# Kernel tuning notes

Measured on AMD Instinct MI355X. Metric: run time of the kernel, lower is better.

The kernel has to match this reference:

```python
import jax, jax.numpy as jnp
import numpy as np
import math

B, T, C = 2, 2048, 1024
H = 16
D = C // H  # 64


def alibi_slopes(n_heads):
    # n_heads is a power of 2 here (16): slopes[i] = start * ratio**i with start==ratio==2**(-8/n)
    start = 2.0 ** (-(2.0 ** (-(math.log2(n_heads) - 3))))
    return jnp.asarray([start * start ** i for i in range(n_heads)], dtype=jnp.float32)


def setup_inputs() -> dict:
    key = jax.random.key(0)
    ks = jax.random.split(key, 6)
    x = jax.random.normal(ks[0], (B, T, C), dtype=jnp.float32)
    W_attn = jax.random.normal(ks[1], (C, 3 * C), dtype=jnp.float32) * 0.02
    b_attn = jnp.zeros((3 * C,), dtype=jnp.float32)
    W_proj = jax.random.normal(ks[2], (C, C), dtype=jnp.float32) * 0.02
    b_proj = jnp.zeros((C,), dtype=jnp.float32)
    temperature = jnp.ones((1,), dtype=jnp.float32) * 2.0
    return {"x": x, "W_attn": W_attn, "b_attn": b_attn,
            "W_proj": W_proj, "b_proj": b_proj, "temperature": temperature}


def reference(x, W_attn, b_attn, W_proj, b_proj, temperature):
    Bc, Tc, Cc = x.shape
    qkv = x @ W_attn + b_attn                      # (B, T, 3C)
    q, k, v = jnp.split(qkv, 3, axis=-1)
    q = q.reshape(Bc, Tc, H, D)
    k = k.reshape(Bc, Tc, H, D)
    v = v.reshape(Bc, Tc, H, D)
    scale = 1.0 / math.sqrt(D)
    att = jnp.einsum('bqhd,bkhd->bhqk', q, k) * scale  # (B, H, T, T)
    att = att / temperature                            # learnable temperature
    # ALiBi bias with causal mask (-inf above diagonal)
    pos = jnp.arange(Tc, dtype=jnp.float32)
    rel = pos[None, :] - pos[:, None]                  # (T, T): memory - context
    slopes = alibi_slopes(H)
    bias = slopes[:, None, None] * rel[None, :, :]
    causal = pos[None, :] <= pos[:, None]              # (T, T) lower-triangular
    bias = jnp.where(causal[None, :, :], bias, -jnp.inf)
    att = att + bias[None, :, :, :]
    w = jax.nn.softmax(att, axis=-1)
    y = jnp.einsum('bhqk,bkhd->bqhd', w, v).reshape(Bc, Tc, Cc)
    return y @ W_proj + b_proj
```

## Files before the change

### kernel.cpp

```cpp
#include <hip/hip_runtime.h>
#include <math.h>

#define B_ 2
#define T_ 2048
#define C_ 1024
#define H_ 16
#define D_ 64
#define M_ (B_*T_)

typedef unsigned short u16;
typedef unsigned int u32;
typedef __attribute__((ext_vector_type(8))) short short8;
typedef __attribute__((ext_vector_type(4))) float f32x4;

__device__ inline u16 f2bf(float f){
  union { float f; unsigned u; } v; v.f = f;
  unsigned r = (v.u + 0x7FFF + ((v.u >> 16) & 1)) >> 16;
  return (u16)r;
}

__device__ inline void gload_lds16(const void* g, void* l){
  __builtin_amdgcn_global_load_lds(
      (const __attribute__((address_space(1))) unsigned*)g,
      (__attribute__((address_space(3))) unsigned*)l, 16, 0, 0);
}

__device__ inline int swzb(int row, int chunk){
  return (row << 7) | ((chunk ^ (row & 7)) << 4);
}

__global__ void k_cvt_x(const float* __restrict__ x, u16* __restrict__ xb){
  int i = (blockIdx.x * 256 + threadIdx.x) * 8;
  float4 a = *(const float4*)(x + i);
  float4 b = *(const float4*)(x + i + 4);
  short8 o;
  o[0] = (short)f2bf(a.x); o[1] = (short)f2bf(a.y);
  o[2] = (short)f2bf(a.z); o[3] = (short)f2bf(a.w);
  o[4] = (short)f2bf(b.x); o[5] = (short)f2bf(b.y);
  o[6] = (short)f2bf(b.z); o[7] = (short)f2bf(b.w);
  *(short8*)(xb + i) = o;
}

__global__ void k_transW(const float* __restrict__ W, u16* __restrict__ Wt, int K, int N){
  __shared__ float t[32][33];
  int bn = blockIdx.x * 32, bk = blockIdx.y * 32;
  int tx = threadIdx.x, ty = threadIdx.y;
  #pragma unroll
  for (int i = 0; i < 32; i += 8)
    t[ty + i][tx] = W[(size_t)(bk + ty + i) * N + bn + tx];
  __syncthreads();
  #pragma unroll
  for (int i = 0; i < 32; i += 8)
    Wt[(size_t)(bn + ty + i) * K + bk + tx] = f2bf(t[tx][ty + i]);
}

__global__ void k_transV(const u16* __restrict__ v, u16* __restrict__ vt){
  __shared__ u16 t[32][33];
  int bh = blockIdx.z;
  int t0 = blockIdx.x * 32, d0 = blockIdx.y * 32;
  int tx = threadIdx.x, ty = threadIdx.y;
  const u16* vs = v + (size_t)bh * T_ * D_;
  u16* vd = vt + (size_t)bh * T_ * D_;
  #pragma unroll
  for (int i = 0; i < 32; i += 8)
    t[ty + i][tx] = vs[(size_t)(t0 + ty + i) * D_ + d0 + tx];
  __syncthreads();
  #pragma unroll
  for (int i = 0; i < 32; i += 8)
    vd[(size_t)(d0 + ty + i) * T_ + t0 + tx] = t[tx][ty + i];
}

template<int EPI>
__launch_bounds__(256, 2)
__global__ void k_gemm(const u16* __restrict__ A, const u16* __restrict__ Bt,
                       const float* __restrict__ bias, float* __restrict__ outF,
                       u16* __restrict__ oq, u16* __restrict__ ok, u16* __restrict__ ov,
                       int M, int N, int K){
  __shared__ u16 lA[128 * 32];
  __shared__ u16 lB[128 * 32];
  int tid = threadIdx.x, lane = tid & 63, wv = tid >> 6;
  int bm = blockIdx.y * 128, bn = blockIdx.x * 128;
  int wr = (wv >> 1) * 64, wc = (wv & 1) * 64;
  f32x4 acc[4][4] = {};

  const u16* Ab = A + (size_t)(bm + wv * 32 + (lane >> 2)) * K + (lane & 3) * 8;
  const u16* Bb = Bt + (size_t)(bn + wv * 32 + (lane >> 2)) * K + (lane & 3) * 8;
  u16* lAd = &lA[wv * 1024];
  u16* lBd = &lB[wv * 1024];
  int ar = wr + (lane & 15);
  int br = wc + (lane & 15);
  int kc = (lane >> 4) * 8;

  for (int k0 = 0; k0 < K; k0 += 32){
    gload_lds16(Ab + k0, lAd);
    gload_lds16(Ab + k0 + (size_t)16 * K, lAd + 512);
    gload_lds16(Bb + k0, lBd);
    gload_lds16(Bb + k0 + (size_t)16 * K, lBd + 512);
    __syncthreads();
    short8 afr[4], bfr[4];
    #pragma unroll
    for (int m = 0; m < 4; m++) afr[m] = *(const short8*)&lA[(ar + m * 16) * 32 + kc];
    #pragma unroll
    for (int n = 0; n < 4; n++) bfr[n] = *(const short8*)&lB[(br + n * 16) * 32 + kc];
    #pragma unroll
    for (int m = 0; m < 4; m++)
      #pragma unroll
      for (int n = 0; n < 4; n++)
        acc[m][n] = __builtin_amdgcn_mfma_f32_16x16x32_bf16(afr[m], bfr[n], acc[m][n], 0, 0, 0);
    __syncthreads();
  }

  if (EPI == 1){
    #pragma unroll
    for (int m = 0; m < 4; m++){
      int gmB = bm + wr + m * 16 + ((lane >> 4) << 2);
      #pragma unroll
      for (int n = 0; n < 4; n++){
        int gn = bn + wc + n * 16 + (lane & 15);
        float bia = bias[gn];
        #pragma unroll
        for (int j = 0; j < 4; j++)
          outF[(size_t)(gmB + j) * N + gn] = acc[m][n][j] + bia;
      }
    }
  } else {
    #pragma unroll
    for (int m = 0; m < 4; m++){
      int gmB = bm + wr + m * 16 + ((lane >> 4) << 2);
      #pragma unroll
      for (int n = 0; n < 4; n++){
        int gn = bn + wc + n * 16 + (lane & 15);
        float bia = bias[gn];
        int part = gn >> 10;
        int col = gn & 1023;
        int h = col >> 6, d = col & 63;
        u16* dst = (part == 0) ? oq : (part == 1) ? ok : ov;
        #pragma unroll
        for (int j = 0; j < 4; j++){
          int gm = gmB + j;
          int b = gm >> 11, t = gm & 2047;
          dst[((size_t)(b * H_ + h) * T_ + t) * D_ + d] = f2bf(acc[m][n][j] + bia);
        }
      }
    }
  }
}

__launch_bounds__(256, 2)
__global__ void k_attn(const u16* __restrict__ q, const u16* __restrict__ k,
                       const u16* __restrict__ vt, u16* __restrict__ y,
                       const float* __restrict__ tempPtr){
  __shared__ u16 lK[64 * 64];
  __shared__ u16 lV[64 * 64];
  __shared__ u16 lP[4][32 * 64];
  const float LOG2E = 1.44269504089f;
  int tid = threadIdx.x, lane = tid & 63, wv = tid >> 6;
  int g = lane >> 4, c = lane & 15;
  int bh = blockIdx.x, h = bh & (H_ - 1), b = bh >> 4;
  int yy = blockIdx.y;
  int qt = (yy & 1) ? ((yy - 1) >> 1) : (15 - (yy >> 1));
  int q0 = qt * 128;
  int qb = q0 + wv * 32;
  float scl2 = LOG2E / (8.0f * tempPtr[0]);
  float slope2 = exp2f(-0.5f * (float)(h + 1)) * LOG2E;
  const u16* qp = q + (size_t)bh * T_ * D_;
  const u16* kp = k + (size_t)bh * T_ * D_;
  const u16* vp = vt + (size_t)bh * T_ * D_;
  char* lKc = (char*)lK;
  char* lVc = (char*)lV;
  char* lPw = (char*)lP[wv];

  short8 qf[2][2];
  #pragma unroll
  for (int m = 0; m < 2; m++)
    #pragma unroll
    for (int ks = 0; ks < 2; ks++)
      qf[m][ks] = *(const short8*)&qp[(size_t)(qb + m * 16 + c) * D_ + ks * 32 + g * 8];

  float boff[16];
  #pragma unroll
  for (int n = 0; n < 4; n++)
    #pragma unroll
    for (int r = 0; r < 4; r++)
      boff[n * 4 + r] = slope2 * (float)(n * 16 + g * 4 + r);
  float sq[2] = { slope2 * (float)(qb + c), slope2 * (float)(qb + 16 + c) };

  float mrun[2] = { -1e30f, -1e30f }, lrun[2] = { 0.f, 0.f };
  f32x4 acco[2][4] = {};

  int sr = tid >> 2, sc = tid & 3;
  const u16* gK = kp + (size_t)sr * D_ + sc * 16;
  const u16* gV = vp + (size_t)sr * T_ + sc * 16;
  short8 rk0, rk1, rv0, rv1;

  int ntiles = (q0 >> 6) + 2;
  int wqmax = qb + 31;

  rk0 = *(const short8*)(gK);     rk1 = *(const short8*)(gK + 8);
  rv0 = *(const short8*)(gV);     rv1 = *(const short8*)(gV + 8);

  for (int t = 0; t < ntiles; t++){
    int kv0 = t << 6;
    __syncthreads();
    *(short8*)(lKc + swzb(sr, sc * 2))     = rk0;
    *(short8*)(lKc + swzb(sr, sc * 2 + 1)) = rk1;
    *(short8*)(lVc + swzb(sr, sc * 2))     = rv0;
    *(short8*)(lVc + swzb(sr, sc * 2 + 1)) = rv1;
    __syncthreads();
    if (t + 1 < ntiles){
      rk0 = *(const short8*)(gK + (t + 1) * 4096);
      rk1 = *(const short8*)(gK + (t + 1) * 4096 + 8);
      rv0 = *(const short8*)(gV + (t + 1) * 64);
      rv1 = *(const short8*)(gV + (t + 1) * 64 + 8);
    }
    if (kv0 > wqmax) continue;

    f32x4 accs[2][4] = {};
    #pragma unroll
    for (int ks = 0; ks < 2; ks++){
      short8 kf[4];
      #pragma unroll
      for (int n = 0; n < 4; n++)
        kf[n] = *(const short8*)(lKc + swzb(n * 16 + c, ks * 4 + g));
      #pragma unroll
      for (int m = 0; m < 2; m++)
        #pragma unroll
        for (int n = 0; n < 4; n++)
          accs[m][n] = __builtin_amdgcn_mfma_f32_16x16x32_bf16(kf[n], qf[m][ks], accs[m][n], 0, 0, 0);
    }

    bool maskt = (kv0 + 64 > qb);
    #pragma unroll
    for (int m = 0; m < 2; m++){
      float b0 = fmaf((float)kv0, slope2, -sq[m]);
      float s[16];
      #pragma unroll
      for (int n = 0; n < 4; n++)
        #pragma unroll
        for (int r = 0; r < 4; r++)
          s[n * 4 + r] = fmaf(accs[m][n][r], scl2, b0 + boff[n * 4 + r]);
      if (maskt){
        int qm = qb + m * 16 + c - kv0;
        #pragma unroll
        for (int n = 0; n < 4; n++)
          #pragma unroll
          for (int r = 0; r < 4; r++)
            s[n * 4 + r] = (n * 16 + g * 4 + r > qm) ? -1e30f : s[n * 4 + r];
      }
      float pm = s[0];
      #pragma unroll
      for (int i = 1; i < 16; i++) pm = fmaxf(pm, s[i]);
      pm = fmaxf(pm, __shfl_xor(pm, 16));
      pm = fmaxf(pm, __shfl_xor(pm, 32));
      if (!__all(pm <= mrun[m] + 8.0f)){
        float nm = fmaxf(mrun[m], pm);
        float al = exp2f(mrun[m] - nm);
        lrun[m] *= al;
        #pragma unroll
        for (int n = 0; n < 4; n++)
          #pragma unroll
          for (int r = 0; r < 4; r++)
            acco[m][n][r] *= al;
        mrun[m] = nm;
      }
      float p[16], ps = 0.f;
      #pragma unroll
      for (int i = 0; i < 16; i++){ p[i] = exp2f(s[i] - mrun[m]); ps += p[i]; }
      lrun[m] += ps;
      #pragma unroll
      for (int n = 0; n < 4; n++){
        u32 w0 = ((u32)f2bf(p[n * 4 + 1]) << 16) | f2bf(p[n * 4 + 0]);
        u32 w1 = ((u32)f2bf(p[n * 4 + 3]) << 16) | f2bf(p[n * 4 + 2]);
        uint2 wp; wp.x = w0; wp.y = w1;
        *(uint2*)(lPw + swzb(c + 16 * m, 2 * n + (g >> 1)) + ((g & 1) << 3)) = wp;
      }
    }

    #pragma unroll
    for (int ks = 0; ks < 2; ks++){
      short8 vf[4], pf[2];
      #pragma unroll
      for (int n = 0; n < 4; n++)
        vf[n] = *(const short8*)(lVc + swzb(n * 16 + c, ks * 4 + g));
      #pragma unroll
      for (int m = 0; m < 2; m++)
        pf[m] = *(const short8*)(lPw + swzb(c + 16 * m, ks * 4 + g));
      #pragma unroll
      for (int m = 0; m < 2; m++)
        #pragma unroll
        for (int n = 0; n < 4; n++)
          acco[m][n] = __builtin_amdgcn_mfma_f32_16x16x32_bf16(vf[n], pf[m], acco[m][n], 0, 0, 0);
    }
  }

  #pragma unroll
  for (int m = 0; m < 2; m++){
    float ls = lrun[m];
    ls += __shfl_xor(ls, 16);
    ls += __shfl_xor(ls, 32);
    float inv = 1.0f / ls;
    int qg = qb + m * 16 + c;
    size_t rowoff = (size_t)(b * T_ + qg) * C_ + h * D_;
    #pragma unroll
    for (int n = 0; n < 4; n++){
      u32 w0 = ((u32)f2bf(acco[m][n][1] * inv) << 16) | f2bf(acco[m][n][0] * inv);
      u32 w1 = ((u32)f2bf(acco[m][n][3] * inv) << 16) | f2bf(acco[m][n][2] * inv);
      uint2 wp; wp.x = w0; wp.y = w1;
      *(uint2*)&y[rowoff + n * 16 + g * 4] = wp;
    }
  }
}

extern "C" void kernel_launch(void* const* d_in, const int* in_sizes, int n_in,
                              void* d_out, int out_size, void* d_ws, size_t ws_size,
                              hipStream_t stream){
  const float* x      = (const float*)d_in[0];
  const float* W_attn = (const float*)d_in[1];
  const float* b_attn = (const float*)d_in[2];
  const float* W_proj = (const float*)d_in[3];
  const float* b_proj = (const float*)d_in[4];
  const float* temp   = (const float*)d_in[5];
  float* out = (float*)d_out;

  if (ws_size < (size_t)41943040) return;
  char* ws = (char*)d_ws;
  u16* xb  = (u16*)(ws);
  u16* wab = (u16*)(ws + 8388608);
  u16* wpt = (u16*)(ws + 14680064);
  u16* qw  = (u16*)(ws + 16777216);
  u16* kw  = (u16*)(ws + 25165824);
  u16* vw  = (u16*)(ws + 33554432);
  u16* vtw = (u16*)(ws);
  u16* yb  = (u16*)(ws + 33554432);

  k_cvt_x<<<2048, 256, 0, stream>>>(x, xb);
  k_transW<<<dim3(96, 32), dim3(32, 8), 0, stream>>>(W_attn, wab, 1024, 3072);
  k_transW<<<dim3(32, 32), dim3(32, 8), 0, stream>>>(W_proj, wpt, 1024, 1024);
  k_gemm<0><<<dim3(24, 32), 256, 0, stream>>>(xb, wab, b_attn, nullptr, qw, kw, vw,
                                              4096, 3072, 1024);
  k_transV<<<dim3(64, 2, 32), dim3(32, 8), 0, stream>>>(vw, vtw);
  k_attn<<<dim3(32, 16), 256, 0, stream>>>(qw, kw, vtw, yb, temp);
  k_gemm<1><<<dim3(8, 32), 256, 0, stream>>>(yb, wpt, b_proj, out, nullptr, nullptr, nullptr,
                                             4096, 1024, 1024);
}
```

Baseline: 231.6 us.

## Split attention into single-wave blocks reading K/V directly, remap GEMM block order

The attention kernel moves from 256-thread blocks sharing K/V tiles through LDS to 64-thread single-wave blocks, each handling 32 query rows and loading K and V fragments straight from global memory. This drops the block-wide barriers and the staged copy pipeline, and gives finer causal load balancing by launching the largest query tiles first. It also rewrites the ALiBi bias arithmetic to use fewer precomputed registers. Separately, the GEMM kernel remaps block IDs into 8 interleaved groups to change cache locality. K/V reuse across waves now relies on L2/L1 caches rather than LDS, which raises global traffic.

```diff
diff --git a/kernel.cpp b/kernel.cpp
--- a/kernel.cpp
+++ b/kernel.cpp
@@ -79,7 +79,10 @@
   __shared__ u16 lA[128 * 32];
   __shared__ u16 lB[128 * 32];
   int tid = threadIdx.x, lane = tid & 63, wv = tid >> 6;
-  int bm = blockIdx.y * 128, bn = blockIdx.x * 128;
+  unsigned nwg = gridDim.x * gridDim.y;
+  unsigned bid = blockIdx.y * gridDim.x + blockIdx.x;
+  unsigned nbid = (bid & 7) * (nwg >> 3) + (bid >> 3);
+  int bm = (int)(nbid / gridDim.x) * 128, bn = (int)(nbid % gridDim.x) * 128;
   int wr = (wv >> 1) * 64, wc = (wv & 1) * 64;
   f32x4 acc[4][4] = {};
 
@@ -146,29 +149,23 @@
   }
 }
 
-__launch_bounds__(256, 2)
+__launch_bounds__(64, 4)
 __global__ void k_attn(const u16* __restrict__ q, const u16* __restrict__ k,
                        const u16* __restrict__ vt, u16* __restrict__ y,
                        const float* __restrict__ tempPtr){
-  __shared__ u16 lK[64 * 64];
-  __shared__ u16 lV[64 * 64];
-  __shared__ u16 lP[4][32 * 64];
+  __shared__ u16 lP[32 * 64];
   const float LOG2E = 1.44269504089f;
-  int tid = threadIdx.x, lane = tid & 63, wv = tid >> 6;
+  int lane = threadIdx.x;
   int g = lane >> 4, c = lane & 15;
   int bh = blockIdx.x, h = bh & (H_ - 1), b = bh >> 4;
-  int yy = blockIdx.y;
-  int qt = (yy & 1) ? ((yy - 1) >> 1) : (15 - (yy >> 1));
-  int q0 = qt * 128;
-  int qb = q0 + wv * 32;
+  int qt = 63 - blockIdx.y;
+  int qb = qt * 32;
   float scl2 = LOG2E / (8.0f * tempPtr[0]);
   float slope2 = exp2f(-0.5f * (float)(h + 1)) * LOG2E;
   const u16* qp = q + (size_t)bh * T_ * D_;
   const u16* kp = k + (size_t)bh * T_ * D_;
   const u16* vp = vt + (size_t)bh * T_ * D_;
-  char* lKc = (char*)lK;
-  char* lVc = (char*)lV;
-  char* lPw = (char*)lP[wv];
+  char* lPw = (char*)lP;
 
   short8 qf[2][2];
   #pragma unroll
@@ -177,43 +174,13 @@
     for (int ks = 0; ks < 2; ks++)
       qf[m][ks] = *(const short8*)&qp[(size_t)(qb + m * 16 + c) * D_ + ks * 32 + g * 8];
 
-  float boff[16];
-  #pragma unroll
-  for (int n = 0; n < 4; n++)
-    #pragma unroll
-    for (int r = 0; r < 4; r++)
-      boff[n * 4 + r] = slope2 * (float)(n * 16 + g * 4 + r);
-  float sq[2] = { slope2 * (float)(qb + c), slope2 * (float)(qb + 16 + c) };
-
+  float dq0 = (float)(g * 4 - c - qb);
   float mrun[2] = { -1e30f, -1e30f }, lrun[2] = { 0.f, 0.f };
   f32x4 acco[2][4] = {};
 
-  int sr = tid >> 2, sc = tid & 3;
-  const u16* gK = kp + (size_t)sr * D_ + sc * 16;
-  const u16* gV = vp + (size_t)sr * T_ + sc * 16;
-  short8 rk0, rk1, rv0, rv1;
-
-  int ntiles = (q0 >> 6) + 2;
-  int wqmax = qb + 31;
-
-  rk0 = *(const short8*)(gK);     rk1 = *(const short8*)(gK + 8);
-  rv0 = *(const short8*)(gV);     rv1 = *(const short8*)(gV + 8);
-
+  int ntiles = (qb + 95) >> 6;
   for (int t = 0; t < ntiles; t++){
     int kv0 = t << 6;
-    __syncthreads();
-    *(short8*)(lKc + swzb(sr, sc * 2))     = rk0;
-    *(short8*)(lKc + swzb(sr, sc * 2 + 1)) = rk1;
-    *(short8*)(lVc + swzb(sr, sc * 2))     = rv0;
-    *(short8*)(lVc + swzb(sr, sc * 2 + 1)) = rv1;
-    __syncthreads();
-    if (t + 1 < ntiles){
-      rk0 = *(const short8*)(gK + (t + 1) * 4096);
-      rk1 = *(const short8*)(gK + (t + 1) * 4096 + 8);
-      rv0 = *(const short8*)(gV + (t + 1) * 64);
-      rv1 = *(const short8*)(gV + (t + 1) * 64 + 8);
-    }
-    if (kv0 > wqmax) continue;
 
     f32x4 accs[2][4] = {};
     #pragma unroll
@@ -221,7 +188,7 @@
       short8 kf[4];
       #pragma unroll
       for (int n = 0; n < 4; n++)
-        kf[n] = *(const short8*)(lKc + swzb(n * 16 + c, ks * 4 + g));
+        kf[n] = *(const short8*)&kp[(size_t)(kv0 + n * 16 + c) * D_ + ks * 32 + g * 8];
       #pragma unroll
       for (int m = 0; m < 2; m++)
         #pragma unroll
@@ -232,20 +199,21 @@
     bool maskt = (kv0 + 64 > qb);
     #pragma unroll
     for (int m = 0; m < 2; m++){
-      float b0 = fmaf((float)kv0, slope2, -sq[m]);
+      float tv = (float)kv0 + dq0 - (float)(16 * m);
       float s[16];
       #pragma unroll
       for (int n = 0; n < 4; n++)
         #pragma unroll
         for (int r = 0; r < 4; r++)
-          s[n * 4 + r] = fmaf(accs[m][n][r], scl2, b0 + boff[n * 4 + r]);
+          s[n * 4 + r] = fmaf(slope2, tv + (float)(n * 16 + r), accs[m][n][r] * scl2);
       if (maskt){
         int qm = qb + m * 16 + c - kv0;
+        int kvg = g * 4;
         #pragma unroll
         for (int n = 0; n < 4; n++)
           #pragma unroll
           for (int r = 0; r < 4; r++)
-            s[n * 4 + r] = (n * 16 + g * 4 + r > qm) ? -1e30f : s[n * 4 + r];
+            s[n * 4 + r] = (n * 16 + kvg + r > qm) ? -1e30f : s[n * 4 + r];
       }
       float pm = s[0];
       #pragma unroll
@@ -281,7 +249,7 @@
       short8 vf[4], pf[2];
       #pragma unroll
       for (int n = 0; n < 4; n++)
-        vf[n] = *(const short8*)(lVc + swzb(n * 16 + c, ks * 4 + g));
+        vf[n] = *(const short8*)&vp[(size_t)(n * 16 + c) * T_ + kv0 + ks * 32 + g * 8];
       #pragma unroll
       for (int m = 0; m < 2; m++)
         pf[m] = *(const short8*)(lPw + swzb(c + 16 * m, ks * 4 + g));
@@ -339,7 +307,7 @@
   k_gemm<0><<<dim3(24, 32), 256, 0, stream>>>(xb, wab, b_attn, nullptr, qw, kw, vw,
                                               4096, 3072, 1024);
   k_transV<<<dim3(64, 2, 32), dim3(32, 8), 0, stream>>>(vw, vtw);
-  k_attn<<<dim3(32, 16), 256, 0, stream>>>(qw, kw, vtw, yb, temp);
+  k_attn<<<dim3(32, 64), 64, 0, stream>>>(qw, kw, vtw, yb, temp);
   k_gemm<1><<<dim3(8, 32), 256, 0, stream>>>(yb, wpt, b_proj, out, nullptr, nullptr, nullptr,
                                              4096, 1024, 1024);
 }
```

New measurement: 268.5 us. 1.16x slower.
